# Kernel optimization log

Measured on AMD Instinct MI355X. Metric: run time of the kernel, lower is better.

Reference implementation:

```python
import jax, jax.numpy as jnp
import numpy as np

D_MODEL, N_HEADS = 768, 12
D_K = D_MODEL // N_HEADS
NEG = -1e9


def setup_inputs() -> dict:
    key = jax.random.key(0)
    ks = jax.random.split(key, 12)
    B, S, D = 2, 4096, D_MODEL
    s = 1.0 / np.sqrt(D)
    inp = {
        'query': jax.random.normal(ks[0], (B, S, D), jnp.float32),
        'key': jax.random.normal(ks[1], (B, S, D), jnp.float32),
        'value': jax.random.normal(ks[2], (B, S, D), jnp.float32),
        'mask': jnp.ones((B, S), jnp.int32),
        'Wq': jax.random.normal(ks[3], (D, D), jnp.float32) * s,
        'bq': jnp.zeros((D,), jnp.float32),
        'Wk': jax.random.normal(ks[4], (D, D), jnp.float32) * s,
        'bk': jnp.zeros((D,), jnp.float32),
        'Wv': jax.random.normal(ks[5], (D, D), jnp.float32) * s,
        'bv': jnp.zeros((D,), jnp.float32),
        'Wo': jax.random.normal(ks[6], (D, D), jnp.float32) * s,
        'bo': jnp.zeros((D,), jnp.float32),
    }
    return inp


def reference(query, key, value, mask, Wq, bq, Wk, bk, Wv, bv, Wo, bo):
    B, Sq, D = query.shape
    Sk = key.shape[1]
    # torch Linear: x @ W.T + b; weights stored [out, in]
    def proj(x, W, b, S):
        return (x @ W.T + b).reshape(B, S, N_HEADS, D_K).transpose(0, 2, 1, 3)
    Q = proj(query, Wq, bq, Sq)   # [B,H,Sq,Dk]
    K = proj(key, Wk, bk, Sk)
    V = proj(value, Wv, bv, Sk)
    scores = jnp.einsum('bhqd,bhkd->bhqk', Q, K) / jnp.sqrt(jnp.float32(D_K))
    # padding mask on keys: [B,1,1,Sk]
    scores = jnp.where(mask[:, None, None, :] == 0, NEG, scores)
    # causal mask (triu, diagonal=1)
    causal = jnp.triu(jnp.ones((Sq, Sk), bool), k=1)
    scores = jnp.where(causal[None, None], NEG, scores)
    attn = jax.nn.softmax(scores, axis=-1)
    out = jnp.einsum('bhqk,bhkd->bhqd', attn, V)
    out = out.transpose(0, 2, 1, 3).reshape(B, Sq, D)
    return out @ Wo.T + bo
```

## Files before the change

### kernel.cpp

```cpp
#include <hip/hip_runtime.h>
#include <hip/hip_bf16.h>

#define D_MODEL 768
#define N_HEADS 12
#define D_K     64
#define NEG_INF (-1e9f)
#define SQ_PAD  72
#define SCALE_Q 0.1803368801111154f
#define W_ELEMS (D_MODEL * D_MODEL)

typedef __attribute__((ext_vector_type(8))) short          bf16x8;
typedef __attribute__((ext_vector_type(4))) float          floatx4;
typedef __attribute__((ext_vector_type(4))) unsigned short ushortx4;
typedef __attribute__((ext_vector_type(2))) unsigned int   uintx2;

static __device__ __forceinline__ unsigned short f2bf(float f) {
    unsigned u = __builtin_bit_cast(unsigned, f);
    u += 0x7FFFu + ((u >> 16) & 1u);
    return (unsigned short)(u >> 16);
}

static __device__ __forceinline__ void gload_lds16(const void* g, void* l) {
    __builtin_amdgcn_global_load_lds(
        (const __attribute__((address_space(1))) void*)g,
        (__attribute__((address_space(3))) void*)l, 16, 0, 0);
}

__global__ __launch_bounds__(256) void convert_w4(
    const float* __restrict__ W0, const float* __restrict__ W1,
    const float* __restrict__ W2, const float* __restrict__ W3,
    unsigned short* __restrict__ out)
{
    const float* src[4] = {W0, W1, W2, W3};
    const float* W = src[blockIdx.y];
    unsigned short* o = out + (size_t)blockIdx.y * W_ELEMS;
    const int i = (blockIdx.x * 256 + threadIdx.x) * 4;
    float4 v = *(const float4*)(W + i);
    ushortx4 h = { f2bf(v.x), f2bf(v.y), f2bf(v.z), f2bf(v.w) };
    *(ushortx4*)(o + i) = h;
}

__global__ __launch_bounds__(256) void convert_a(
    const float* __restrict__ A, unsigned short* __restrict__ out)
{
    const int i = (blockIdx.x * 256 + threadIdx.x) * 4;
    float4 v = *(const float4*)(A + i);
    ushortx4 h = { f2bf(v.x), f2bf(v.y), f2bf(v.z), f2bf(v.w) };
    *(ushortx4*)(out + i) = h;
}

template <int MODE>
__global__ __launch_bounds__(256) void gemm_bt(
    const unsigned short* __restrict__ A, const unsigned short* __restrict__ Bm,
    const float* __restrict__ bias, void* __restrict__ Cout,
    int M, int N, int K, int S)
{
    __shared__ __align__(16) unsigned short As[64 * 64];
    __shared__ __align__(16) unsigned short Bs[128 * 64];

    const int tid  = threadIdx.x;
    const int wave = tid >> 6;
    const int lane = tid & 63;
    const int quad = lane >> 4;
    const int l16  = lane & 15;
    const int r8   = lane >> 3;
    const int c8   = (lane & 7) << 3;
    const int m0 = blockIdx.x * 64;
    const int n0 = blockIdx.y * 128;
    const int wm = (wave & 1) * 32;
    const int wn = (wave >> 1) * 64;

    const floatx4 zero4 = {0.f, 0.f, 0.f, 0.f};
    floatx4 acc[2][4];
    #pragma unroll
    for (int i = 0; i < 2; ++i)
        #pragma unroll
        for (int j = 0; j < 4; ++j) acc[i][j] = zero4;

    for (int k0 = 0; k0 < K; k0 += 64) {
        #pragma unroll
        for (int c = 0; c < 2; ++c) {
            const int row = wave * 16 + c * 8;
            gload_lds16(A + (size_t)(m0 + row + r8) * K + k0 + c8,
                        As + row * 64);
        }
        #pragma unroll
        for (int c = 0; c < 4; ++c) {
            const int row = wave * 32 + c * 8;
            gload_lds16(Bm + (size_t)(n0 + row + r8) * K + k0 + c8,
                        Bs + row * 64);
        }
        __syncthreads();

        bf16x8 af[2][2], bfr[2][4];
        #pragma unroll
        for (int kh = 0; kh < 2; ++kh) {
            #pragma unroll
            for (int i = 0; i < 2; ++i)
                af[kh][i] = *(const bf16x8*)(As + (wm + i * 16 + l16) * 64 + kh * 32 + quad * 8);
            #pragma unroll
            for (int j = 0; j < 4; ++j)
                bfr[kh][j] = *(const bf16x8*)(Bs + (wn + j * 16 + l16) * 64 + kh * 32 + quad * 8);
        }
        #pragma unroll
        for (int kh = 0; kh < 2; ++kh)
            #pragma unroll
            for (int i = 0; i < 2; ++i)
                #pragma unroll
                for (int j = 0; j < 4; ++j)
                    acc[i][j] = __builtin_amdgcn_mfma_f32_16x16x32_bf16(
                        af[kh][i], bfr[kh][j], acc[i][j], 0, 0, 0);
        __syncthreads();
    }

    #pragma unroll
    for (int i = 0; i < 2; ++i) {
        #pragma unroll
        for (int j = 0; j < 4; ++j) {
            const int col = n0 + wn + j * 16 + l16;
            const float bv = bias[col];
            if constexpr (MODE == 3) {
                const int t0 = m0 + wm + i * 16 + quad * 4;
                const int b  = t0 / S;
                const int s0 = t0 - b * S;
                const int hh = col >> 6, d = col & 63;
                ushortx4 hv;
                #pragma unroll
                for (int r = 0; r < 4; ++r) hv[r] = f2bf(acc[i][j][r] + bv);
                *(ushortx4*)((unsigned short*)Cout +
                    ((size_t)(b * N_HEADS + hh) * D_K + d) * S + s0) = hv;
            } else {
                #pragma unroll
                for (int r = 0; r < 4; ++r) {
                    const int row = m0 + wm + i * 16 + quad * 4 + r;
                    float v = acc[i][j][r] + bv;
                    if constexpr (MODE == 2) v *= SCALE_Q;
                    if constexpr (MODE == 0)
                        ((float*)Cout)[(size_t)row * N + col] = v;
                    else
                        ((unsigned short*)Cout)[(size_t)row * N + col] = f2bf(v);
                }
            }
        }
    }
}

__global__ __launch_bounds__(256) void flash_attn(
    const unsigned short* __restrict__ Qp,
    const unsigned short* __restrict__ Kp,
    const unsigned short* __restrict__ VpT,
    const int* __restrict__ mask,
    unsigned short* __restrict__ O,
    int S)
{
    __shared__ __align__(16) unsigned short Ks [64 * SQ_PAD];
    __shared__ __align__(16) unsigned short Vts[64 * SQ_PAD];
    __shared__ __align__(16) unsigned short Ps [4][16 * SQ_PAD];
    __shared__ __align__(16) float mskf[64];

    const int L  = blockIdx.x;
    const int bh = L % 24;
    const int p  = L / 24;
    const int h  = bh % 12;
    const int b  = bh / 12;
    const int nqt = S >> 6;
    const int tid  = threadIdx.x;
    const int wave = tid >> 6;
    const int lane = tid & 63;
    const int quad = lane >> 4;
    const int l16  = lane & 15;

    const unsigned short* Kbase = Kp  + (size_t)(b * S) * D_MODEL + h * D_K;
    const unsigned short* Vbase = VpT + (size_t)(b * N_HEADS + h) * D_K * S;

    const floatx4 zero4 = {0.f, 0.f, 0.f, 0.f};
    const short one_bf = (short)0x3F80;
    const bf16x8 ones = {one_bf, one_bf, one_bf, one_bf,
                         one_bf, one_bf, one_bf, one_bf};

    #pragma unroll
    for (int sel = 0; sel < 2; ++sel) {
        const int qt = sel ? (nqt - 1 - p) : p;
        const int q0 = qt * 64;
        const int qbase = q0 + wave * 16;

        const size_t rowQ = (size_t)(b * S + qbase + l16) * D_MODEL + h * D_K;
        const bf16x8 qf0 = *(const bf16x8*)(Qp + rowQ + quad * 8);
        const bf16x8 qf1 = *(const bf16x8*)(Qp + rowQ + 32 + quad * 8);

        floatx4 acc2[4];
        floatx4 acc_l = zero4;
        #pragma unroll
        for (int dt = 0; dt < 4; ++dt) acc2[dt] = zero4;

        for (int kt = 0; kt <= qt; ++kt) {
            const int k0 = kt * 64;
            #pragma unroll
            for (int g = tid; g < 512; g += 256) {
                const int row = g >> 3, cg = (g & 7) << 3;
                *(bf16x8*)(Ks + row * SQ_PAD + cg) =
                    *(const bf16x8*)(Kbase + (size_t)(k0 + row) * D_MODEL + cg);
                *(bf16x8*)(Vts + row * SQ_PAD + cg) =
                    *(const bf16x8*)(Vbase + (size_t)row * S + k0 + cg);
            }
            if (tid < 64)
                mskf[tid] = (mask[b * S + k0 + tid] == 0) ? NEG_INF : 0.f;
            __syncthreads();

            floatx4 s[4];
            #pragma unroll
            for (int nt = 0; nt < 4; ++nt) {
                floatx4 c = *(const floatx4*)(mskf + nt * 16 + quad * 4);
                bf16x8 kf0 = *(const bf16x8*)(Ks + (nt * 16 + l16) * SQ_PAD + quad * 8);
                bf16x8 kf1 = *(const bf16x8*)(Ks + (nt * 16 + l16) * SQ_PAD + 32 + quad * 8);
                c = __builtin_amdgcn_mfma_f32_16x16x32_bf16(kf0, qf0, c, 0, 0, 0);
                c = __builtin_amdgcn_mfma_f32_16x16x32_bf16(kf1, qf1, c, 0, 0, 0);
                s[nt] = c;
            }

            if (kt == qt) {
                const int qrel = wave * 16 + l16;
                #pragma unroll
                for (int nt = 0; nt < 4; ++nt) {
                    const int krel = nt * 16 + quad * 4;
                    #pragma unroll
                    for (int r = 0; r < 4; ++r)
                        if (krel + r > qrel) s[nt][r] = NEG_INF;
                }
            }

            #pragma unroll
            for (int nt = 0; nt < 4; ++nt) {
                const float e0 = __builtin_exp2f(s[nt][0]);
                const float e1 = __builtin_exp2f(s[nt][1]);
                const float e2 = __builtin_exp2f(s[nt][2]);
                const float e3 = __builtin_exp2f(s[nt][3]);
                uintx2 pk;
                pk[0] = __builtin_amdgcn_perm(__builtin_bit_cast(unsigned, e1),
                                              __builtin_bit_cast(unsigned, e0), 0x07060302u);
                pk[1] = __builtin_amdgcn_perm(__builtin_bit_cast(unsigned, e3),
                                              __builtin_bit_cast(unsigned, e2), 0x07060302u);
                *(uintx2*)(Ps[wave] + l16 * SQ_PAD + nt * 16 + quad * 4) = pk;
            }

            #pragma unroll
            for (int kh = 0; kh < 2; ++kh) {
                bf16x8 pf = *(const bf16x8*)(Ps[wave] + l16 * SQ_PAD + kh * 32 + quad * 8);
                #pragma unroll
                for (int dt = 0; dt < 4; ++dt) {
                    bf16x8 vf = *(const bf16x8*)(Vts + (dt * 16 + l16) * SQ_PAD + kh * 32 + quad * 8);
                    acc2[dt] = __builtin_amdgcn_mfma_f32_16x16x32_bf16(pf, vf, acc2[dt], 0, 0, 0);
                }
                acc_l = __builtin_amdgcn_mfma_f32_16x16x32_bf16(pf, ones, acc_l, 0, 0, 0);
            }
            __syncthreads();
        }

        #pragma unroll
        for (int r = 0; r < 4; ++r) {
            const float inv = 1.f / acc_l[r];
            const int gq = qbase + quad * 4 + r;
            const size_t base = (size_t)(b * S + gq) * D_MODEL + h * D_K;
            #pragma unroll
            for (int dt = 0; dt < 4; ++dt)
                O[base + dt * 16 + l16] = f2bf(acc2[dt][r] * inv);
        }
        __syncthreads();
    }
}

extern "C" void kernel_launch(void* const* d_in, const int* in_sizes, int n_in,
                              void* d_out, int out_size, void* d_ws, size_t ws_size,
                              hipStream_t stream) {
    const float* query = (const float*)d_in[0];
    const float* key   = (const float*)d_in[1];
    const float* value = (const float*)d_in[2];
    const int*   mask  = (const int*)d_in[3];
    const float* Wq = (const float*)d_in[4];
    const float* bq = (const float*)d_in[5];
    const float* Wk = (const float*)d_in[6];
    const float* bk = (const float*)d_in[7];
    const float* Wv = (const float*)d_in[8];
    const float* bv = (const float*)d_in[9];
    const float* Wo = (const float*)d_in[10];
    const float* bo = (const float*)d_in[11];

    const int B  = 2;
    const int BS = in_sizes[3];
    const int S  = BS / B;
    const int M  = BS;

    unsigned short* Qp  = (unsigned short*)d_ws;
    unsigned short* Kp  = Qp  + (size_t)M * D_MODEL;
    unsigned short* VpT = Kp  + (size_t)M * D_MODEL;
    unsigned short* Obf = VpT + (size_t)M * D_MODEL;
    unsigned short* Wbf = Obf + (size_t)M * D_MODEL;
    unsigned short* Wqb = Wbf;
    unsigned short* Wkb = Wbf + (size_t)W_ELEMS;
    unsigned short* Wvb = Wbf + (size_t)W_ELEMS * 2;
    unsigned short* Wob = Wbf + (size_t)W_ELEMS * 3;

    dim3 blk(256);
    const int actblocks = (M * D_MODEL) / 1024;
    convert_w4<<<dim3(W_ELEMS / 1024, 4), blk, 0, stream>>>(Wq, Wk, Wv, Wo, Wbf);

    dim3 ggrid(M / 64, D_MODEL / 128);
    convert_a<<<actblocks, blk, 0, stream>>>(query, Obf);
    gemm_bt<2><<<ggrid, blk, 0, stream>>>(Obf, Wqb, bq, Qp,  M, D_MODEL, D_MODEL, S);
    convert_a<<<actblocks, blk, 0, stream>>>(key, Obf);
    gemm_bt<1><<<ggrid, blk, 0, stream>>>(Obf, Wkb, bk, Kp,  M, D_MODEL, D_MODEL, S);
    convert_a<<<actblocks, blk, 0, stream>>>(value, Obf);
    gemm_bt<3><<<ggrid, blk, 0, stream>>>(Obf, Wvb, bv, VpT, M, D_MODEL, D_MODEL, S);

    flash_attn<<<768, blk, 0, stream>>>(Qp, Kp, VpT, mask, Obf, S);

    gemm_bt<0><<<ggrid, blk, 0, stream>>>(Obf, Wob, bo, (float*)d_out, M, D_MODEL, D_MODEL, S);
}
```

Baseline: 347.8 us.

## Batch QKV projections into one launch, enlarge GEMM and attention key tiles

Merges the three activation conversions and the three QKV projection GEMMs into single batched launches indexed by blockIdx, using d_out as scratch for the converted key and value. The GEMM moves to 128x128 tiles with K-step 32 and transposed MFMA operands so each lane writes four contiguous outputs. Flash attention now processes 128-key tiles per iteration with wider padded V/P buffers. The intent is fewer launches, more reuse per tile and fewer sync points, at the cost of more LDS and registers and extra causal work on the final 128-key tile.

```diff
diff --git a/kernel.cpp b/kernel.cpp
--- a/kernel.cpp
+++ b/kernel.cpp
@@ -5,7 +5,8 @@
 #define N_HEADS 12
 #define D_K     64
 #define NEG_INF (-1e9f)
-#define SQ_PAD  72
+#define KS_PAD  72
+#define VT_PAD  136
 #define SCALE_Q 0.1803368801111154f
 #define W_ELEMS (D_MODEL * D_MODEL)
 
@@ -40,106 +41,115 @@
     *(ushortx4*)(o + i) = h;
 }
 
-__global__ __launch_bounds__(256) void convert_a(
-    const float* __restrict__ A, unsigned short* __restrict__ out)
+__global__ __launch_bounds__(256) void convert_a3(
+    const float* __restrict__ A0, const float* __restrict__ A1,
+    const float* __restrict__ A2,
+    unsigned short* __restrict__ O0, unsigned short* __restrict__ O1,
+    unsigned short* __restrict__ O2)
 {
+    const int z = blockIdx.y;
+    const float* A = (z == 0) ? A0 : (z == 1) ? A1 : A2;
+    unsigned short* O = (z == 0) ? O0 : (z == 1) ? O1 : O2;
     const int i = (blockIdx.x * 256 + threadIdx.x) * 4;
     float4 v = *(const float4*)(A + i);
     ushortx4 h = { f2bf(v.x), f2bf(v.y), f2bf(v.z), f2bf(v.w) };
-    *(ushortx4*)(out + i) = h;
-}
-
-template <int MODE>
-__global__ __launch_bounds__(256) void gemm_bt(
-    const unsigned short* __restrict__ A, const unsigned short* __restrict__ Bm,
-    const float* __restrict__ bias, void* __restrict__ Cout,
-    int M, int N, int K, int S)
+    *(ushortx4*)(O + i) = h;
+}
+
+template <bool QKV>
+__global__ __launch_bounds__(256) void gemm128(
+    const unsigned short* __restrict__ A0, const unsigned short* __restrict__ A1,
+    const unsigned short* __restrict__ A2,
+    const unsigned short* __restrict__ W0, const unsigned short* __restrict__ W1,
+    const unsigned short* __restrict__ W2,
+    const float* __restrict__ b0, const float* __restrict__ b1,
+    const float* __restrict__ b2,
+    void* __restrict__ C0, void* __restrict__ C1, void* __restrict__ C2,
+    int S)
 {
-    __shared__ __align__(16) unsigned short As[64 * 64];
-    __shared__ __align__(16) unsigned short Bs[128 * 64];
+    __shared__ __align__(16) unsigned short As[128 * 32];
+    __shared__ __align__(16) unsigned short Bs[128 * 32];
+
+    const int z = QKV ? blockIdx.z : 0;
+    const unsigned short* A = (z == 0) ? A0 : (z == 1) ? A1 : A2;
+    const unsigned short* W = (z == 0) ? W0 : (z == 1) ? W1 : W2;
+    const float* bias       = (z == 0) ? b0 : (z == 1) ? b1 : b2;
+    void* C                 = (z == 0) ? C0 : (z == 1) ? C1 : C2;
+    const float scale = (QKV && z == 0) ? SCALE_Q : 1.0f;
+    const int mode = QKV ? ((z == 2) ? 3 : 1) : 0;
 
     const int tid  = threadIdx.x;
     const int wave = tid >> 6;
     const int lane = tid & 63;
     const int quad = lane >> 4;
     const int l16  = lane & 15;
-    const int r8   = lane >> 3;
-    const int c8   = (lane & 7) << 3;
-    const int m0 = blockIdx.x * 64;
+    const int m0 = blockIdx.x * 128;
     const int n0 = blockIdx.y * 128;
-    const int wm = (wave & 1) * 32;
+    const int wm = (wave & 1) * 64;
     const int wn = (wave >> 1) * 64;
+    const int sr = lane >> 2;
+    const int sc = (lane & 3) << 3;
 
     const floatx4 zero4 = {0.f, 0.f, 0.f, 0.f};
-    floatx4 acc[2][4];
+    floatx4 acc[4][4];
     #pragma unroll
-    for (int i = 0; i < 2; ++i)
+    for (int i = 0; i < 4; ++i)
         #pragma unroll
         for (int j = 0; j < 4; ++j) acc[i][j] = zero4;
 
-    for (int k0 = 0; k0 < K; k0 += 64) {
+    for (int k0 = 0; k0 < D_MODEL; k0 += 32) {
         #pragma unroll
         for (int c = 0; c < 2; ++c) {
-            const int row = wave * 16 + c * 8;
-            gload_lds16(A + (size_t)(m0 + row + r8) * K + k0 + c8,
-                        As + row * 64);
-        }
-        #pragma unroll
-        for (int c = 0; c < 4; ++c) {
-            const int row = wave * 32 + c * 8;
-            gload_lds16(Bm + (size_t)(n0 + row + r8) * K + k0 + c8,
-                        Bs + row * 64);
+            const int row = wave * 32 + c * 16;
+            gload_lds16(A + (size_t)(m0 + row + sr) * D_MODEL + k0 + sc,
+                        As + row * 32);
+            gload_lds16(W + (size_t)(n0 + row + sr) * D_MODEL + k0 + sc,
+                        Bs + row * 32);
         }
         __syncthreads();
 
-        bf16x8 af[2][2], bfr[2][4];
-        #pragma unroll
-        for (int kh = 0; kh < 2; ++kh) {
-            #pragma unroll
-            for (int i = 0; i < 2; ++i)
-                af[kh][i] = *(const bf16x8*)(As + (wm + i * 16 + l16) * 64 + kh * 32 + quad * 8);
+        bf16x8 af[4], bfr[4];
+        #pragma unroll
+        for (int i = 0; i < 4; ++i)
+            af[i] = *(const bf16x8*)(As + (wm + i * 16 + l16) * 32 + quad * 8);
+        #pragma unroll
+        for (int j = 0; j < 4; ++j)
+            bfr[j] = *(const bf16x8*)(Bs + (wn + j * 16 + l16) * 32 + quad * 8);
+        #pragma unroll
+        for (int i = 0; i < 4; ++i)
             #pragma unroll
             for (int j = 0; j < 4; ++j)
-                bfr[kh][j] = *(const bf16x8*)(Bs + (wn + j * 16 + l16) * 64 + kh * 32 + quad * 8);
-        }
-        #pragma unroll
-        for (int kh = 0; kh < 2; ++kh)
-            #pragma unroll
-            for (int i = 0; i < 2; ++i)
-                #pragma unroll
-                for (int j = 0; j < 4; ++j)
-                    acc[i][j] = __builtin_amdgcn_mfma_f32_16x16x32_bf16(
-                        af[kh][i], bfr[kh][j], acc[i][j], 0, 0, 0);
+                acc[i][j] = __builtin_amdgcn_mfma_f32_16x16x32_bf16(
+                    bfr[j], af[i], acc[i][j], 0, 0, 0);
         __syncthreads();
     }
 
     #pragma unroll
-    for (int i = 0; i < 2; ++i) {
+    for (int i = 0; i < 4; ++i) {
+        const int m = m0 + wm + i * 16 + l16;
         #pragma unroll
         for (int j = 0; j < 4; ++j) {
-            const int col = n0 + wn + j * 16 + l16;
-            const float bv = bias[col];
-            if constexpr (MODE == 3) {
-                const int t0 = m0 + wm + i * 16 + quad * 4;
-                const int b  = t0 / S;
-                const int s0 = t0 - b * S;
-                const int hh = col >> 6, d = col & 63;
-                ushortx4 hv;
-                #pragma unroll
-                for (int r = 0; r < 4; ++r) hv[r] = f2bf(acc[i][j][r] + bv);
-                *(ushortx4*)((unsigned short*)Cout +
-                    ((size_t)(b * N_HEADS + hh) * D_K + d) * S + s0) = hv;
+            const int nb = n0 + wn + j * 16 + quad * 4;
+            const float4 bv = *(const float4*)(bias + nb);
+            float v0 = (acc[i][j][0] + bv.x) * scale;
+            float v1 = (acc[i][j][1] + bv.y) * scale;
+            float v2 = (acc[i][j][2] + bv.z) * scale;
+            float v3 = (acc[i][j][3] + bv.w) * scale;
+            if (mode == 0) {
+                float4 o = {v0, v1, v2, v3};
+                *(float4*)((float*)C + (size_t)m * D_MODEL + nb) = o;
+            } else if (mode == 1) {
+                ushortx4 o = {f2bf(v0), f2bf(v1), f2bf(v2), f2bf(v3)};
+                *(ushortx4*)((unsigned short*)C + (size_t)m * D_MODEL + nb) = o;
             } else {
-                #pragma unroll
-                for (int r = 0; r < 4; ++r) {
-                    const int row = m0 + wm + i * 16 + quad * 4 + r;
-                    float v = acc[i][j][r] + bv;
-                    if constexpr (MODE == 2) v *= SCALE_Q;
-                    if constexpr (MODE == 0)
-                        ((float*)Cout)[(size_t)row * N + col] = v;
-                    else
-                        ((unsigned short*)Cout)[(size_t)row * N + col] = f2bf(v);
-                }
+                const int bb = m / S, s = m - bb * S;
+                const int hh = nb >> 6, d = nb & 63;
+                unsigned short* base = (unsigned short*)C +
+                    ((size_t)(bb * N_HEADS + hh) * D_K + d) * S + s;
+                base[0]         = f2bf(v0);
+                base[(size_t)S]     = f2bf(v1);
+                base[(size_t)S * 2] = f2bf(v2);
+                base[(size_t)S * 3] = f2bf(v3);
             }
         }
     }
@@ -153,10 +163,10 @@
     unsigned short* __restrict__ O,
     int S)
 {
-    __shared__ __align__(16) unsigned short Ks [64 * SQ_PAD];
-    __shared__ __align__(16) unsigned short Vts[64 * SQ_PAD];
-    __shared__ __align__(16) unsigned short Ps [4][16 * SQ_PAD];
-    __shared__ __align__(16) float mskf[64];
+    __shared__ __align__(16) unsigned short Ks [128 * KS_PAD];
+    __shared__ __align__(16) unsigned short Vts[64 * VT_PAD];
+    __shared__ __align__(16) unsigned short Ps [4][16 * VT_PAD];
+    __shared__ __align__(16) float mskf[128];
 
     const int L  = blockIdx.x;
     const int bh = L % 24;
@@ -183,6 +193,7 @@
         const int qt = sel ? (nqt - 1 - p) : p;
         const int q0 = qt * 64;
         const int qbase = q0 + wave * 16;
+        const int qabs = qbase + l16;
 
         const size_t rowQ = (size_t)(b * S + qbase + l16) * D_MODEL + h * D_K;
         const bf16x8 qf0 = *(const bf16x8*)(Qp + rowQ + quad * 8);
@@ -193,44 +204,45 @@
         #pragma unroll
         for (int dt = 0; dt < 4; ++dt) acc2[dt] = zero4;
 
-        for (int kt = 0; kt <= qt; ++kt) {
-            const int k0 = kt * 64;
-            #pragma unroll
-            for (int g = tid; g < 512; g += 256) {
-                const int row = g >> 3, cg = (g & 7) << 3;
-                *(bf16x8*)(Ks + row * SQ_PAD + cg) =
-                    *(const bf16x8*)(Kbase + (size_t)(k0 + row) * D_MODEL + cg);
-                *(bf16x8*)(Vts + row * SQ_PAD + cg) =
-                    *(const bf16x8*)(Vbase + (size_t)row * S + k0 + cg);
-            }
-            if (tid < 64)
+        const int ni = (qt >> 1) + 1;
+        for (int kt = 0; kt < ni; ++kt) {
+            const int k0 = kt * 128;
+            #pragma unroll
+            for (int g = tid; g < 1024; g += 256) {
+                const int krow = g >> 3, kc = (g & 7) << 3;
+                *(bf16x8*)(Ks + krow * KS_PAD + kc) =
+                    *(const bf16x8*)(Kbase + (size_t)(k0 + krow) * D_MODEL + kc);
+                const int vrow = g >> 4, vc = (g & 15) << 3;
+                *(bf16x8*)(Vts + vrow * VT_PAD + vc) =
+                    *(const bf16x8*)(Vbase + (size_t)vrow * S + k0 + vc);
+            }
+            if (tid < 128)
                 mskf[tid] = (mask[b * S + k0 + tid] == 0) ? NEG_INF : 0.f;
             __syncthreads();
 
-            floatx4 s[4];
-            #pragma unroll
-            for (int nt = 0; nt < 4; ++nt) {
+            floatx4 s[8];
+            #pragma unroll
+            for (int nt = 0; nt < 8; ++nt) {
                 floatx4 c = *(const floatx4*)(mskf + nt * 16 + quad * 4);
-                bf16x8 kf0 = *(const bf16x8*)(Ks + (nt * 16 + l16) * SQ_PAD + quad * 8);
-                bf16x8 kf1 = *(const bf16x8*)(Ks + (nt * 16 + l16) * SQ_PAD + 32 + quad * 8);
+                bf16x8 kf0 = *(const bf16x8*)(Ks + (nt * 16 + l16) * KS_PAD + quad * 8);
+                bf16x8 kf1 = *(const bf16x8*)(Ks + (nt * 16 + l16) * KS_PAD + 32 + quad * 8);
                 c = __builtin_amdgcn_mfma_f32_16x16x32_bf16(kf0, qf0, c, 0, 0, 0);
                 c = __builtin_amdgcn_mfma_f32_16x16x32_bf16(kf1, qf1, c, 0, 0, 0);
                 s[nt] = c;
             }
 
-            if (kt == qt) {
-                const int qrel = wave * 16 + l16;
+            if (kt == ni - 1) {
                 #pragma unroll
-                for (int nt = 0; nt < 4; ++nt) {
-                    const int krel = nt * 16 + quad * 4;
+                for (int nt = 0; nt < 8; ++nt) {
+                    const int kb = k0 + nt * 16 + quad * 4;
                     #pragma unroll
                     for (int r = 0; r < 4; ++r)
-                        if (krel + r > qrel) s[nt][r] = NEG_INF;
+                        if (kb + r > qabs) s[nt][r] = NEG_INF;
                 }
             }
 
             #pragma unroll
-            for (int nt = 0; nt < 4; ++nt) {
+            for (int nt = 0; nt < 8; ++nt) {
                 const float e0 = __builtin_exp2f(s[nt][0]);
                 const float e1 = __builtin_exp2f(s[nt][1]);
                 const float e2 = __builtin_exp2f(s[nt][2]);
@@ -240,15 +252,15 @@
                                               __builtin_bit_cast(unsigned, e0), 0x07060302u);
                 pk[1] = __builtin_amdgcn_perm(__builtin_bit_cast(unsigned, e3),
                                               __builtin_bit_cast(unsigned, e2), 0x07060302u);
-                *(uintx2*)(Ps[wave] + l16 * SQ_PAD + nt * 16 + quad * 4) = pk;
-            }
-
-            #pragma unroll
-            for (int kh = 0; kh < 2; ++kh) {
-                bf16x8 pf = *(const bf16x8*)(Ps[wave] + l16 * SQ_PAD + kh * 32 + quad * 8);
+                *(uintx2*)(Ps[wave] + l16 * VT_PAD + nt * 16 + quad * 4) = pk;
+            }
+
+            #pragma unroll
+            for (int kh = 0; kh < 4; ++kh) {
+                bf16x8 pf = *(const bf16x8*)(Ps[wave] + l16 * VT_PAD + kh * 32 + quad * 8);
                 #pragma unroll
                 for (int dt = 0; dt < 4; ++dt) {
-                    bf16x8 vf = *(const bf16x8*)(Vts + (dt * 16 + l16) * SQ_PAD + kh * 32 + quad * 8);
+                    bf16x8 vf = *(const bf16x8*)(Vts + (dt * 16 + l16) * VT_PAD + kh * 32 + quad * 8);
                     acc2[dt] = __builtin_amdgcn_mfma_f32_16x16x32_bf16(pf, vf, acc2[dt], 0, 0, 0);
                 }
                 acc_l = __builtin_amdgcn_mfma_f32_16x16x32_bf16(pf, ones, acc_l, 0, 0, 0);
@@ -299,20 +311,20 @@
     unsigned short* Wkb = Wbf + (size_t)W_ELEMS;
     unsigned short* Wvb = Wbf + (size_t)W_ELEMS * 2;
     unsigned short* Wob = Wbf + (size_t)W_ELEMS * 3;
+    unsigned short* ka = (unsigned short*)d_out;
+    unsigned short* va = ka + (size_t)M * D_MODEL;
 
     dim3 blk(256);
-    const int actblocks = (M * D_MODEL) / 1024;
     convert_w4<<<dim3(W_ELEMS / 1024, 4), blk, 0, stream>>>(Wq, Wk, Wv, Wo, Wbf);
-
-    dim3 ggrid(M / 64, D_MODEL / 128);
-    convert_a<<<actblocks, blk, 0, stream>>>(query, Obf);
-    gemm_bt<2><<<ggrid, blk, 0, stream>>>(Obf, Wqb, bq, Qp,  M, D_MODEL, D_MODEL, S);
-    convert_a<<<actblocks, blk, 0, stream>>>(key, Obf);
-    gemm_bt<1><<<ggrid, blk, 0, stream>>>(Obf, Wkb, bk, Kp,  M, D_MODEL, D_MODEL, S);
-    convert_a<<<actblocks, blk, 0, stream>>>(value, Obf);
-    gemm_bt<3><<<ggrid, blk, 0, stream>>>(Obf, Wvb, bv, VpT, M, D_MODEL, D_MODEL, S);
+    convert_a3<<<dim3((M * D_MODEL) / 1024, 3), blk, 0, stream>>>(
+        query, key, value, Obf, ka, va);
+
+    gemm128<true><<<dim3(M / 128, D_MODEL / 128, 3), blk, 0, stream>>>(
+        Obf, ka, va, Wqb, Wkb, Wvb, bq, bk, bv, Qp, Kp, VpT, S);
 
     flash_attn<<<768, blk, 0, stream>>>(Qp, Kp, VpT, mask, Obf, S);
 
-    gemm_bt<0><<<ggrid, blk, 0, stream>>>(Obf, Wob, bo, (float*)d_out, M, D_MODEL, D_MODEL, S);
-}
+    gemm128<false><<<dim3(M / 128, D_MODEL / 128, 1), blk, 0, stream>>>(
+        Obf, Obf, Obf, Wob, Wob, Wob, bo, bo, bo,
+        d_out, d_out, d_out, S);
+}
```

Result: faster. 319.6 us (-8.1%).
